# Optimization experiments

Hardware: AMD Instinct MI355X
Metric: run time of the kernel (lower is better)

Reference implementation:

```python
import jax, jax.numpy as jnp
import numpy as np

# Clos factorization for in=out=4096, middle_switch_multiplier=4:
BIN, B1, B2, B3, BOUT = 64, 64, 256, 64, 64
B, C, D = 2, 4096, 4096


def setup_inputs() -> dict:
    key = jax.random.key(0)
    ks = jax.random.split(key, 7)
    k = 1.0 / np.sqrt(D)
    x = jax.random.normal(ks[0], (B, C, D), dtype=jnp.float32)
    # kaiming_uniform(a=sqrt(5)) on [bin,b1,b2]-like tensors ~ uniform(-bound, bound)
    w1 = jax.random.uniform(ks[1], (BIN, B1, B2), jnp.float32, -k, k)
    w2 = jax.random.uniform(ks[2], (B1, B2, B3), jnp.float32, -k, k)
    w3 = jax.random.uniform(ks[3], (B2, B3, BOUT), jnp.float32, -k, k)
    bias1 = jax.random.uniform(ks[4], (B1,), jnp.float32, -k, k)
    bias2 = jax.random.uniform(ks[5], (B2,), jnp.float32, -k, k)
    bias3 = jax.random.uniform(ks[6], (B3,), jnp.float32, -k, k)
    return {"x": x, "w1": w1, "w2": w2, "w3": w3,
            "bias1": bias1, "bias2": bias2, "bias3": bias3}


def reference(x, w1, w2, w3, bias1, bias2, bias3):
    b, c, _ = x.shape
    h = x.reshape(b, c, BIN, B1)                      # [b,c,n=bin,r=b1]
    h = jnp.einsum('bcnr,nrm->bcmr', h, w1) + bias1   # [b,c,b2,b1] + bias over b1
    h = jnp.einsum('bcmr,rmn->bcnm', h, w2) + bias2   # [b,c,b3,b2] + bias over b2
    h = jnp.einsum('bcnm,mro->bcor', h, w3) + bias3   # [b,c,bout,b3] + bias over b3
    return h.reshape(b, c, -1)                        # [b,c,out_features]
```

## Files before the change

kernel.cpp:

```cpp
#include <hip/hip_runtime.h>
#include <stdint.h>
#include <stddef.h>

typedef __bf16 bf16_t;
typedef __bf16 bf16x8 __attribute__((ext_vector_type(8)));
typedef __bf16 bf16x4 __attribute__((ext_vector_type(4)));
typedef float f32x4 __attribute__((ext_vector_type(4)));

__device__ __forceinline__ void gload_lds16(const void* g, void* l) {
  __builtin_amdgcn_global_load_lds(
      (const __attribute__((address_space(1))) uint32_t*)g,
      (__attribute__((address_space(3))) uint32_t*)l, 16, 0, 0);
}

__global__ void prep1_k(const float* __restrict__ w2, const float* __restrict__ w3,
                        float* __restrict__ w2s, bf16_t* __restrict__ w3pt) {
  __shared__ float lds[64][65];
  const int b = blockIdx.x;
  const int t = threadIdx.x;
  if (b < 64) {
    const int r = b, m = t;
    const float4* p = (const float4*)(w2 + ((size_t)(r * 256 + m)) * 64);
    float s = 0.f;
#pragma unroll
    for (int i = 0; i < 16; ++i) {
      float4 v = p[i];
      s += (v.x + v.y) + (v.z + v.w);
    }
    w2s[r * 256 + m] = s;
    return;
  }
  const int b2 = b - 64;
  const int r = b2 & 63;
  const int mt = (b2 >> 6) * 64;
#pragma unroll
  for (int it = 0; it < 16; ++it) {
    int idx = t + it * 256;
    int ml = idx >> 6, o = idx & 63;
    lds[ml][o] = w3[(size_t)(mt + ml) * 4096 + r * 64 + o];
  }
  __syncthreads();
#pragma unroll
  for (int it = 0; it < 16; ++it) {
    int idx = t + it * 256;
    int o = idx >> 6, ml = idx & 63;
    w3pt[(size_t)(o * 64 + r) * 256 + mt + ml] = (bf16_t)lds[ml][o];
  }
}

__global__ void prep2_k(const float* __restrict__ w1, const float* __restrict__ w2s,
                        const float* __restrict__ bias1, const float* __restrict__ bias2,
                        bf16_t* __restrict__ w1t, float* __restrict__ c2) {
  __shared__ float lds[64][65];
  const int b = blockIdx.x;
  const int t = threadIdx.x;
  if (b == 256) {
    float s = 64.f * bias2[t];
#pragma unroll 8
    for (int r = 0; r < 64; ++r) s += bias1[r] * w2s[r * 256 + t];
    c2[t] = s;
    return;
  }
  const int k0 = (b >> 2) * 64;
  const int mt = (b & 3) * 64;
#pragma unroll
  for (int it = 0; it < 16; ++it) {
    int idx = t + it * 256;
    int kl = idx >> 6, ml = idx & 63;
    int k = k0 + kl;
    lds[kl][ml] = w1[(size_t)k * 256 + mt + ml] * w2s[(k & 63) * 256 + mt + ml];
  }
  __syncthreads();
#pragma unroll
  for (int it = 0; it < 16; ++it) {
    int idx = t + it * 256;
    int ml = idx >> 6, kl = idx & 63;
    w1t[(size_t)(mt + ml) * 4096 + k0 + kl] = (bf16_t)lds[kl][ml];
  }
}

__global__ __launch_bounds__(512, 1) void gemm1_k(
    const float* __restrict__ X, const bf16_t* __restrict__ W1T,
    bf16_t* __restrict__ S4) {
  __shared__ __align__(16) bf16_t lA[2][64 * 64];
  __shared__ __align__(16) bf16_t lB[2][256 * 64];
  const int tid = threadIdx.x;
  const int lane = tid & 63;
  const int wv = tid >> 6;
  const int mtile = (int)blockIdx.x >> 2;
  const int kh = (int)blockIdx.x & 3;
  const size_t m0 = (size_t)mtile * 64;
  const int kbase = kh * 1024;
  const int wm = wv >> 2, wn = wv & 3;
  const int r0 = tid >> 4;
  const int f4 = tid & 15;

  f32x4 acc[2][4];
#pragma unroll
  for (int i = 0; i < 2; ++i)
#pragma unroll
    for (int j = 0; j < 4; ++j) acc[i][j] = (f32x4){0.f, 0.f, 0.f, 0.f};

  float4 aReg[2];

  auto issueA = [&](int kt) {
#pragma unroll
    for (int p = 0; p < 2; ++p) {
      int row = r0 + p * 32;
      aReg[p] = *(const float4*)(X + (m0 + row) * 4096 + (size_t)(kbase + kt * 64 + f4 * 4));
    }
  };
  auto writeA = [&](int buf) {
#pragma unroll
    for (int p = 0; p < 2; ++p) {
      int row = r0 + p * 32;
      int off = row * 128 + ((f4 * 8) ^ ((row & 7) << 4));
      bf16x4 v;
      v[0] = (bf16_t)aReg[p].x;
      v[1] = (bf16_t)aReg[p].y;
      v[2] = (bf16_t)aReg[p].z;
      v[3] = (bf16_t)aReg[p].w;
      *(bf16x4*)((char*)(&lA[buf][0]) + off) = v;
    }
  };
  auto issueB = [&](int buf, int kt) {
#pragma unroll
    for (int i = 0; i < 4; ++i) {
      int row = wv * 32 + i * 8 + (lane >> 3);
      int srckb = ((lane & 7) * 16) ^ ((row & 7) << 4);
      const char* src = (const char*)W1T + (size_t)row * 8192 + (size_t)(kbase + kt * 64) * 2 + srckb;
      char* dst = (char*)(&lB[buf][0]) + (wv * 32 + i * 8) * 128;
      gload_lds16(src, dst);
    }
  };
  auto compute = [&](int buf) {
#pragma unroll
    for (int kk = 0; kk < 2; ++kk) {
      const int kb = kk * 64 + ((lane >> 4) * 16);
      bf16x8 af[2], bfr[4];
#pragma unroll
      for (int mf = 0; mf < 2; ++mf) {
        int row = wm * 32 + mf * 16 + (lane & 15);
        int off = row * 128 + (kb ^ ((row & 7) << 4));
        af[mf] = *(const bf16x8*)((const char*)(&lA[buf][0]) + off);
      }
#pragma unroll
      for (int nf = 0; nf < 4; ++nf) {
        int row = wn * 64 + nf * 16 + (lane & 15);
        int off = row * 128 + (kb ^ ((row & 7) << 4));
        bfr[nf] = *(const bf16x8*)((const char*)(&lB[buf][0]) + off);
      }
#pragma unroll
      for (int mf = 0; mf < 2; ++mf)
#pragma unroll
        for (int nf = 0; nf < 4; ++nf)
          acc[mf][nf] = __builtin_amdgcn_mfma_f32_16x16x32_bf16(af[mf], bfr[nf], acc[mf][nf], 0, 0, 0);
    }
  };

  issueA(0);
  issueB(0, 0);
  writeA(0);
  __syncthreads();
#pragma unroll 1
  for (int kt = 0; kt < 16; ++kt) {
    int cur = kt & 1;
    bool more = (kt + 1) < 16;
    if (more) {
      issueA(kt + 1);
      issueB(cur ^ 1, kt + 1);
    }
    compute(cur);
    if (more) writeA(cur ^ 1);
    __syncthreads();
  }

#pragma unroll
  for (int nf = 0; nf < 4; ++nf) {
    int col = wn * 64 + nf * 16 + (lane & 15);
#pragma unroll
    for (int mf = 0; mf < 2; ++mf) {
#pragma unroll
      for (int q = 0; q < 4; ++q) {
        int row = wm * 32 + mf * 16 + (lane >> 4) * 4 + q;
        S4[(m0 + row) * 1024 + (size_t)(kh * 256 + col)] = (bf16_t)acc[mf][nf][q];
      }
    }
  }
}

__global__ void reduce_k(const bf16_t* __restrict__ S4, const float* __restrict__ c2,
                         bf16_t* __restrict__ S) {
  int gid = blockIdx.x * 256 + threadIdx.x;
  int row = gid >> 5;
  int c8 = (gid & 31) << 3;
  float s[8];
  float4 ca = *(const float4*)(c2 + c8);
  float4 cb = *(const float4*)(c2 + c8 + 4);
  s[0] = ca.x; s[1] = ca.y; s[2] = ca.z; s[3] = ca.w;
  s[4] = cb.x; s[5] = cb.y; s[6] = cb.z; s[7] = cb.w;
#pragma unroll
  for (int h = 0; h < 4; ++h) {
    bf16x8 v = *(const bf16x8*)(S4 + (size_t)row * 1024 + h * 256 + c8);
#pragma unroll
    for (int j = 0; j < 8; ++j) s[j] += (float)v[j];
  }
  bf16x8 o;
#pragma unroll
  for (int j = 0; j < 8; ++j) o[j] = (bf16_t)s[j];
  *(bf16x8*)(S + (size_t)row * 256 + c8) = o;
}

__global__ __launch_bounds__(512, 1) void gemm2_k(
    const bf16_t* __restrict__ S, const bf16_t* __restrict__ W3pT,
    const float* __restrict__ bias3, float* __restrict__ OUT) {
  __shared__ __align__(16) bf16_t lA[2][128 * 64];
  __shared__ __align__(16) bf16_t lB[2][128 * 64];
  const int tid = threadIdx.x;
  const int lane = tid & 63;
  const int wv = tid >> 6;
  const int mt = (int)blockIdx.x >> 5;
  const int nt = (int)blockIdx.x & 31;
  const size_t m0 = (size_t)mt * 128;
  const int n0 = nt * 128;
  const int wm = wv >> 2, wn = wv & 3;

  f32x4 acc[4][2];
#pragma unroll
  for (int i = 0; i < 4; ++i)
#pragma unroll
    for (int j = 0; j < 2; ++j) acc[i][j] = (f32x4){0.f, 0.f, 0.f, 0.f};

  auto stage = [&](int buf, int kt) {
#pragma unroll
    for (int p = 0; p < 2; ++p) {
      int row = wv * 8 + (lane >> 3) + p * 64;
      int srckb = ((lane & 7) * 16) ^ ((row & 7) << 4);
      const char* srcA = (const char*)S + (m0 + row) * 512 + (size_t)(kt * 128 + srckb);
      char* dstA = (char*)(&lA[buf][0]) + (wv * 8 + p * 64) * 128;
      gload_lds16(srcA, dstA);
      const char* srcB = (const char*)W3pT + (size_t)(n0 + row) * 512 + (size_t)(kt * 128 + srckb);
      char* dstB = (char*)(&lB[buf][0]) + (wv * 8 + p * 64) * 128;
      gload_lds16(srcB, dstB);
    }
  };
  auto compute = [&](int buf) {
#pragma unroll
    for (int kk = 0; kk < 2; ++kk) {
      const int kb = kk * 64 + ((lane >> 4) * 16);
      bf16x8 af[4], bfr[2];
#pragma unroll
      for (int mf = 0; mf < 4; ++mf) {
        int row = wm * 64 + mf * 16 + (lane & 15);
        int off = row * 128 + (kb ^ ((row & 7) << 4));
        af[mf] = *(const bf16x8*)((const char*)(&lA[buf][0]) + off);
      }
#pragma unroll
      for (int nf = 0; nf < 2; ++nf) {
        int row = wn * 32 + nf * 16 + (lane & 15);
        int off = row * 128 + (kb ^ ((row & 7) << 4));
        bfr[nf] = *(const bf16x8*)((const char*)(&lB[buf][0]) + off);
      }
#pragma unroll
      for (int mf = 0; mf < 4; ++mf)
#pragma unroll
        for (int nf = 0; nf < 2; ++nf)
          acc[mf][nf] = __builtin_amdgcn_mfma_f32_16x16x32_bf16(af[mf], bfr[nf], acc[mf][nf], 0, 0, 0);
    }
  };

  stage(0, 0);
  __syncthreads();
#pragma unroll 1
  for (int kt = 0; kt < 4; ++kt) {
    int cur = kt & 1;
    if (kt + 1 < 4) stage(cur ^ 1, kt + 1);
    compute(cur);
    __syncthreads();
  }

#pragma unroll
  for (int nf = 0; nf < 2; ++nf) {
    int jcol = wn * 32 + nf * 16 + (lane & 15);
    float b3 = bias3[jcol & 63];
    int j = n0 + jcol;
#pragma unroll
    for (int mf = 0; mf < 4; ++mf) {
#pragma unroll
      for (int q = 0; q < 4; ++q) {
        size_t row = m0 + (size_t)(wm * 64 + mf * 16 + (lane >> 4) * 4 + q);
        OUT[row * 4096 + j] = acc[mf][nf][q] + b3;
      }
    }
  }
}

extern "C" void kernel_launch(void* const* d_in, const int* in_sizes, int n_in,
                              void* d_out, int out_size, void* d_ws, size_t ws_size,
                              hipStream_t stream) {
  (void)in_sizes; (void)n_in; (void)out_size; (void)ws_size;
  const float* x  = (const float*)d_in[0];
  const float* w1 = (const float*)d_in[1];
  const float* w2 = (const float*)d_in[2];
  const float* w3 = (const float*)d_in[3];
  const float* b1 = (const float*)d_in[4];
  const float* b2 = (const float*)d_in[5];
  const float* b3 = (const float*)d_in[6];
  float* out = (float*)d_out;
  char* ws = (char*)d_ws;

  float*  w2s  = (float*)(ws + 0);
  float*  c2   = (float*)(ws + 65536);
  bf16_t* w1t  = (bf16_t*)(ws + 69632);
  bf16_t* w3pt = (bf16_t*)(ws + 69632 + 2097152);
  bf16_t* S4   = (bf16_t*)(ws + 69632 + 2 * 2097152);
  bf16_t* S    = (bf16_t*)(ws + 69632 + 2 * 2097152 + 16777216);

  prep1_k<<<320, 256, 0, stream>>>(w2, w3, w2s, w3pt);
  prep2_k<<<257, 256, 0, stream>>>(w1, w2s, b1, b2, w1t, c2);
  gemm1_k<<<512, 512, 0, stream>>>(x, w1t, S4);
  reduce_k<<<1024, 256, 0, stream>>>(S4, c2, S);
  gemm2_k<<<2048, 512, 0, stream>>>(S, w3pt, b3, out);
}
```

Baseline: 103.5 us.

## Prefetch A two tiles ahead, raise occupancy hints, remap gemm2 blocks across XCDs

The gemm1 loop is unrolled by two with two register buffers for X, so global loads for tile k+2 are in flight while tile k is computed. The A conversion and LDS write now happen after compute instead of stalling on a fresh load. Both GEMMs raise the launch-bounds min-blocks hint to 4 to allow more resident blocks per CU, at the cost of register pressure. gemm2 also remaps block IDs in groups of 8 so that consecutive tiles land on the same XCD, aiming for better L2 reuse.

New measurement: 106.0 us. +2.4%, slower.

```diff
diff --git a/kernel.cpp b/kernel.cpp
--- a/kernel.cpp
+++ b/kernel.cpp
@@ -79,7 +79,7 @@
   }
 }
 
-__global__ __launch_bounds__(512, 1) void gemm1_k(
+__global__ __launch_bounds__(512, 4) void gemm1_k(
     const float* __restrict__ X, const bf16_t* __restrict__ W1T,
     bf16_t* __restrict__ S4) {
   __shared__ __align__(16) bf16_t lA[2][64 * 64];
@@ -101,25 +101,25 @@
 #pragma unroll
     for (int j = 0; j < 4; ++j) acc[i][j] = (f32x4){0.f, 0.f, 0.f, 0.f};
 
-  float4 aReg[2];
-
-  auto issueA = [&](int kt) {
+  float4 aR0[2], aR1[2];
+
+  auto issueA = [&](float4 (&dst)[2], int kt) {
 #pragma unroll
     for (int p = 0; p < 2; ++p) {
       int row = r0 + p * 32;
-      aReg[p] = *(const float4*)(X + (m0 + row) * 4096 + (size_t)(kbase + kt * 64 + f4 * 4));
-    }
-  };
-  auto writeA = [&](int buf) {
+      dst[p] = *(const float4*)(X + (m0 + row) * 4096 + (size_t)(kbase + kt * 64 + f4 * 4));
+    }
+  };
+  auto writeA = [&](const float4 (&src)[2], int buf) {
 #pragma unroll
     for (int p = 0; p < 2; ++p) {
       int row = r0 + p * 32;
       int off = row * 128 + ((f4 * 8) ^ ((row & 7) << 4));
       bf16x4 v;
-      v[0] = (bf16_t)aReg[p].x;
-      v[1] = (bf16_t)aReg[p].y;
-      v[2] = (bf16_t)aReg[p].z;
-      v[3] = (bf16_t)aReg[p].w;
+      v[0] = (bf16_t)src[p].x;
+      v[1] = (bf16_t)src[p].y;
+      v[2] = (bf16_t)src[p].z;
+      v[3] = (bf16_t)src[p].w;
       *(bf16x4*)((char*)(&lA[buf][0]) + off) = v;
     }
   };
@@ -158,20 +158,22 @@
     }
   };
 
-  issueA(0);
+  issueA(aR0, 0);
   issueB(0, 0);
-  writeA(0);
+  writeA(aR0, 0);
+  issueA(aR1, 1);
   __syncthreads();
 #pragma unroll 1
-  for (int kt = 0; kt < 16; ++kt) {
-    int cur = kt & 1;
-    bool more = (kt + 1) < 16;
-    if (more) {
-      issueA(kt + 1);
-      issueB(cur ^ 1, kt + 1);
-    }
-    compute(cur);
-    if (more) writeA(cur ^ 1);
+  for (int kt2 = 0; kt2 < 16; kt2 += 2) {
+    if (kt2 + 1 < 16) issueB(1, kt2 + 1);
+    compute(0);
+    if (kt2 + 1 < 16) writeA(aR1, 1);
+    if (kt2 + 2 < 16) issueA(aR0, kt2 + 2);
+    __syncthreads();
+    if (kt2 + 2 < 16) issueB(0, kt2 + 2);
+    compute(1);
+    if (kt2 + 2 < 16) writeA(aR0, 0);
+    if (kt2 + 3 < 16) issueA(aR1, kt2 + 3);
     __syncthreads();
   }
 
@@ -189,8 +191,9 @@
   }
 }
 
-__global__ void reduce_k(const bf16_t* __restrict__ S4, const float* __restrict__ c2,
-                         bf16_t* __restrict__ S) {
+__global__ __launch_bounds__(256) void reduce_k(
+    const bf16_t* __restrict__ S4, const float* __restrict__ c2,
+    bf16_t* __restrict__ S) {
   int gid = blockIdx.x * 256 + threadIdx.x;
   int row = gid >> 5;
   int c8 = (gid & 31) << 3;
@@ -211,7 +214,7 @@
   *(bf16x8*)(S + (size_t)row * 256 + c8) = o;
 }
 
-__global__ __launch_bounds__(512, 1) void gemm2_k(
+__global__ __launch_bounds__(512, 4) void gemm2_k(
     const bf16_t* __restrict__ S, const bf16_t* __restrict__ W3pT,
     const float* __restrict__ bias3, float* __restrict__ OUT) {
   __shared__ __align__(16) bf16_t lA[2][128 * 64];
@@ -219,8 +222,10 @@
   const int tid = threadIdx.x;
   const int lane = tid & 63;
   const int wv = tid >> 6;
-  const int mt = (int)blockIdx.x >> 5;
-  const int nt = (int)blockIdx.x & 31;
+  const int bid = (int)blockIdx.x;
+  const int newbid = (bid & 7) * 256 + (bid >> 3);
+  const int mt = newbid >> 5;
+  const int nt = newbid & 31;
   const size_t m0 = (size_t)mt * 128;
   const int n0 = nt * 128;
   const int wm = wv >> 2, wn = wv & 3;
```
